# Kernel tuning notes

Hardware: AMD Instinct MI355X
Metric: run time of the kernel (lower is better)

Reference implementation:

```python
import jax, jax.numpy as jnp
import numpy as np

H = 1024      # hidden_size
I = 4096      # intermediate_size
E = 8         # num_experts
TOP_K = 2
LB_COEF = 0.01


def setup_inputs() -> dict:
    key = jax.random.key(0)
    ks = jax.random.split(key, 8)
    s_h = 1.0 / np.sqrt(H)
    s_i = 1.0 / np.sqrt(I)
    return {
        "x": jax.random.normal(ks[0], (2, 2048, H), dtype=jnp.float32),
        "Wr": jax.random.normal(ks[1], (H, E), dtype=jnp.float32) * s_h,
        "br": jnp.zeros((E,), dtype=jnp.float32),
        "W1": jax.random.normal(ks[2], (E, H, I), dtype=jnp.float32) * s_h,
        "b1": jnp.zeros((E, I), dtype=jnp.float32),
        "W2": jax.random.normal(ks[3], (E, I, H), dtype=jnp.float32) * s_i,
        "b2": jnp.zeros((E, H), dtype=jnp.float32),
    }


def _moe_forward(x, Wr, br, W1, b1, W2, b2):
    B, S, Hd = x.shape
    x_flat = x.reshape(-1, Hd)                      # [T, H]
    T = x_flat.shape[0]

    # ---- Router: softmax probs, top-k, renormalize ----
    logits = x_flat @ Wr + br                       # [T, E]
    probs = jax.nn.softmax(logits, axis=-1)         # [T, E]
    topk_w, topk_idx = jax.lax.top_k(probs, TOP_K)  # [T, K]
    topk_w = topk_w / jnp.sum(topk_w, axis=-1, keepdims=True)

    # ---- Load-balance aux loss (switch-style) ----
    onehot = jax.nn.one_hot(topk_idx, E, dtype=x.dtype)   # [T, K, E]
    frac_tokens = onehot.mean(axis=(0, 1))                 # [E]
    frac_probs = probs.mean(axis=0)                        # [E]
    aux_loss = E * jnp.sum(frac_tokens * frac_probs) * LB_COEF

    # combine_weights[t, e] = routing weight of expert e for token t (0 if unselected)
    combine = jnp.sum(topk_w[..., None] * onehot, axis=1)  # [T, E]

    # ---- Experts: dense per-expert FFN, weighted combine ----
    out = jnp.zeros_like(x_flat)
    for e in range(E):
        h = jax.nn.gelu(x_flat @ W1[e] + b1[e])            # [T, I]
        y = h @ W2[e] + b2[e]                              # [T, H]
        out = out + y * combine[:, e:e + 1]
    return out.reshape(B, S, Hd), aux_loss


def reference(x, Wr, br, W1, b1, W2, b2):
    return _moe_forward(x, Wr, br, W1, b1, W2, b2)
```

## Files before the change

### kernel.cpp

```cpp
#include <hip/hip_runtime.h>
#include <hip/hip_bf16.h>

#define HD 1024
#define ID 4096
#define NE 8
#define NT 4096
#define NSLOT (NT*2)

typedef __attribute__((ext_vector_type(4))) float f32x4;
typedef __attribute__((ext_vector_type(8))) short bf16x8;
typedef __attribute__((ext_vector_type(4))) unsigned int u32x4;
typedef __attribute__((ext_vector_type(2))) unsigned int u32x2;
typedef unsigned short u16;

__device__ __forceinline__ u16 f2b(float f) {
  __hip_bfloat16 h = __float2bfloat16(f);
  return __builtin_bit_cast(unsigned short, h);
}
__device__ __forceinline__ unsigned int pack2(float a, float b) {
  return (unsigned int)f2b(a) | ((unsigned int)f2b(b) << 16);
}
__device__ __forceinline__ void gload16(const void* g, void* l) {
  __builtin_amdgcn_global_load_lds(
      (const __attribute__((address_space(1))) unsigned int*)g,
      (__attribute__((address_space(3))) unsigned int*)l, 16, 0, 0);
}
__device__ __forceinline__ float gelu_tanh(float v) {
  float c = v + 0.044715f * v * v * v;
  return 0.5f * v * (1.0f + tanhf(0.7978845608028654f * c));
}

__global__ void k_convert_x(const float* __restrict__ x, u16* __restrict__ xb) {
  int i = blockIdx.x * 256 + threadIdx.x;
  const f32x4* x4 = (const f32x4*)x;
  f32x4 a = x4[2 * i], b = x4[2 * i + 1];
  u32x4 r;
  r[0] = pack2(a[0], a[1]); r[1] = pack2(a[2], a[3]);
  r[2] = pack2(b[0], b[1]); r[3] = pack2(b[2], b[3]);
  ((u32x4*)xb)[i] = r;
}

__global__ __launch_bounds__(256) void k_transpose_bf16(
    const float* __restrict__ src, u16* __restrict__ dst, int R, int C) {
  __shared__ float tile[64][65];
  int e = blockIdx.z;
  int c0 = blockIdx.x * 64;
  int r0 = blockIdx.y * 64;
  int t = threadIdx.x;
  const float* s = src + (size_t)e * R * C;
#pragma unroll
  for (int i = 0; i < 16; ++i) {
    int r = i * 4 + (t >> 6);
    tile[r][t & 63] = s[(size_t)(r0 + r) * C + c0 + (t & 63)];
  }
  __syncthreads();
  u16* d = dst + (size_t)e * R * C;
#pragma unroll
  for (int i = 0; i < 4; ++i) {
    int c = i * 16 + (t >> 4);
    int rb = (t & 15) * 4;
    u32x2 p;
    p[0] = pack2(tile[rb + 0][c], tile[rb + 1][c]);
    p[1] = pack2(tile[rb + 2][c], tile[rb + 3][c]);
    *(u32x2*)&d[(size_t)(c0 + c) * R + r0 + rb] = p;
  }
}

__global__ __launch_bounds__(256) void k_router(
    const float* __restrict__ x, const float* __restrict__ Wr,
    const float* __restrict__ br, int* __restrict__ cnt,
    int* __restrict__ slotE, int* __restrict__ slotLoc,
    float* __restrict__ slotW, float* __restrict__ probsAll) {
  __shared__ float wrt[NE * HD];
  int t = threadIdx.x;
  for (int i = t; i < NE * HD; i += 256) wrt[(i & 7) * HD + (i >> 3)] = Wr[i];
  __syncthreads();
  int wave = t >> 6, lane = t & 63;
  int token = blockIdx.x * 4 + wave;
  const float* xr = x + (size_t)token * HD;
  float acc[NE] = {0, 0, 0, 0, 0, 0, 0, 0};
#pragma unroll 4
  for (int j = 0; j < 16; ++j) {
    int h = j * 64 + lane;
    float xv = xr[h];
#pragma unroll
    for (int e = 0; e < NE; ++e) acc[e] += xv * wrt[e * HD + h];
  }
#pragma unroll
  for (int d = 1; d < 64; d <<= 1) {
#pragma unroll
    for (int e = 0; e < NE; ++e) acc[e] += __shfl_xor(acc[e], d, 64);
  }
  if (lane == 0) {
    float lg[NE], p[NE];
    float m = -1e30f;
#pragma unroll
    for (int e = 0; e < NE; ++e) { lg[e] = acc[e] + br[e]; m = fmaxf(m, lg[e]); }
    float s = 0.f;
#pragma unroll
    for (int e = 0; e < NE; ++e) { p[e] = expf(lg[e] - m); s += p[e]; }
    float inv = 1.0f / s;
    int i1 = 0, i2 = -1;
    float v1 = -1.f, v2 = -1.f;
#pragma unroll
    for (int e = 0; e < NE; ++e) {
      p[e] *= inv;
      probsAll[token * NE + e] = p[e];
      if (p[e] > v1) { v2 = v1; i2 = i1; v1 = p[e]; i1 = e; }
      else if (p[e] > v2) { v2 = p[e]; i2 = e; }
    }
    float wsum = v1 + v2;
    int l1 = atomicAdd(&cnt[i1], 1);
    int l2 = atomicAdd(&cnt[i2], 1);
    slotE[token * 2] = i1;     slotLoc[token * 2] = l1;     slotW[token * 2] = v1 / wsum;
    slotE[token * 2 + 1] = i2; slotLoc[token * 2 + 1] = l2; slotW[token * 2 + 1] = v2 / wsum;
  }
}

__global__ __launch_bounds__(256) void k_psum(const float* __restrict__ probsAll,
                                              float* __restrict__ psumG) {
  __shared__ float red[256];
  int t = threadIdx.x;
  int base = blockIdx.x * 128;
  float s = 0.f;
  for (int i = t >> 3; i < 128; i += 32) s += probsAll[(base + i) * NE + (t & 7)];
  red[t] = s;
  __syncthreads();
  for (int st = 128; st >= 8; st >>= 1) {
    if (t < st) red[t] += red[t + st];
    __syncthreads();
  }
  if (t < 8) atomicAdd(&psumG[t], red[t]);
}

__global__ void k_finalize(const float* __restrict__ psumG, const int* __restrict__ cnt,
                           int* __restrict__ off, float* __restrict__ out_aux) {
  if (threadIdx.x == 0) {
    int o = 0;
    float a = 0.f;
    for (int e = 0; e < NE; ++e) {
      off[e] = o;
      o += cnt[e];
      a += ((float)cnt[e] / (float)NSLOT) * (psumG[e] / (float)NT);
    }
    off[NE] = o;
    out_aux[0] = (float)NE * a * 0.01f;
  }
}

__global__ void k_scatter(const int* __restrict__ slotE, const int* __restrict__ slotLoc,
                          const float* __restrict__ slotW, const int* __restrict__ off,
                          int* __restrict__ rowTok, float* __restrict__ rowW) {
  int i = blockIdx.x * 256 + threadIdx.x;
  int pos = off[slotE[i]] + slotLoc[i];
  if (pos < 0) pos = 0;
  if (pos >= NSLOT) pos = NSLOT - 1;
  rowTok[pos] = i >> 1;
  rowW[pos] = slotW[i];
}

#define STG(bf) do { \
    _Pragma("unroll") \
    for (int i_ = 0; i_ < 4; ++i_) { \
      gload16(aSrc[i_], &As[bf][dstc[i_]]); \
      gload16(bSrc[i_], &Bs[bf][dstc[i_]]); \
      aSrc[i_] += 64; bSrc[i_] += 64; \
    } \
  } while (0)

__global__ __launch_bounds__(512, 1) void k_gemm1(
    const u16* __restrict__ xb, const u16* __restrict__ w1t,
    const float* __restrict__ b1, u16* __restrict__ hbuf,
    const int* __restrict__ cnt, const int* __restrict__ off,
    const int* __restrict__ rowTok) {
  int bid = blockIdx.x;
  int e = bid >> 8;
  int m0 = ((bid >> 4) & 15) * 256;
  int n0 = (bid & 15) * 256;
  int ce = cnt[e];
  if (m0 >= ce) return;
  int oe = off[e];
  __shared__ u16 As[2][256 * 64];
  __shared__ u16 Bs[2][256 * 64];
  __shared__ int rtok[256];
  int t = threadIdx.x;
  if (t < 256) {
    int r = m0 + t;
    if (r >= ce) r = ce - 1;
    int tok = rowTok[oe + r];
    rtok[t] = (tok < 0) ? 0 : (tok >= NT ? NT - 1 : tok);
  }
  __syncthreads();
  const u16* aSrc[4];
  const u16* bSrc[4];
  int dstc[4];
  const u16* bb = w1t + (size_t)e * ID * HD + (size_t)n0 * HD;
#pragma unroll
  for (int i = 0; i < 4; ++i) {
    int c = t + 512 * i;
    int row = c >> 3, slot = c & 7, j = slot ^ (row & 7);
    aSrc[i] = xb + (size_t)rtok[row] * HD + j * 8;
    bSrc[i] = bb + (size_t)row * HD + j * 8;
    dstc[i] = c * 8;
  }
  int lane = t & 63, wave = t >> 6;
  int wr = wave >> 2, wc = wave & 3;
  f32x4 acc[8][4] = {};
  const int NK = HD / 64;
  STG(0);
  STG(1);
  for (int kt = 0; kt < NK; ++kt) {
    if (kt + 1 < NK) asm volatile("s_waitcnt vmcnt(8)" ::: "memory");
    else             asm volatile("s_waitcnt vmcnt(0)" ::: "memory");
    __builtin_amdgcn_s_barrier();
    int cb = kt & 1;
#pragma unroll
    for (int kk = 0; kk < 2; ++kk) {
      bf16x8 af[8], bv[4];
#pragma unroll
      for (int mm = 0; mm < 8; ++mm) {
        int ra = wr * 128 + mm * 16 + (lane & 15);
        int slot = (kk * 4 + (lane >> 4)) ^ (ra & 7);
        af[mm] = *(const bf16x8*)&As[cb][ra * 64 + slot * 8];
      }
#pragma unroll
      for (int nn = 0; nn < 4; ++nn) {
        int rb = wc * 64 + nn * 16 + (lane & 15);
        int slot = (kk * 4 + (lane >> 4)) ^ (rb & 7);
        bv[nn] = *(const bf16x8*)&Bs[cb][rb * 64 + slot * 8];
      }
#pragma unroll
      for (int mm = 0; mm < 8; ++mm)
#pragma unroll
        for (int nn = 0; nn < 4; ++nn)
          acc[mm][nn] = __builtin_amdgcn_mfma_f32_16x16x32_bf16(af[mm], bv[nn], acc[mm][nn], 0, 0, 0);
    }
    if (kt + 2 < NK) {
      __builtin_amdgcn_s_barrier();
      STG(kt & 1);
    }
  }
  const float* b1e = b1 + (size_t)e * ID + n0;
#pragma unroll
  for (int nn = 0; nn < 4; ++nn) {
    int col = wc * 64 + nn * 16 + (lane & 15);
    float bias = b1e[col];
#pragma unroll
    for (int mm = 0; mm < 8; ++mm) {
      int lr0 = wr * 128 + mm * 16 + (lane >> 4) * 4;
#pragma unroll
      for (int r = 0; r < 4; ++r) {
        int grow = m0 + lr0 + r;
        if (grow < ce) {
          float v = acc[mm][nn][r] + bias;
          hbuf[(size_t)(oe + grow) * ID + n0 + col] = f2b(gelu_tanh(v));
        }
      }
    }
  }
}

__global__ __launch_bounds__(512, 1) void k_gemm2(
    const u16* __restrict__ hbuf, const u16* __restrict__ w2t,
    const float* __restrict__ b2, float* __restrict__ out,
    const int* __restrict__ cnt, const int* __restrict__ off,
    const int* __restrict__ rowTok, const float* __restrict__ rowW) {
  int bid = blockIdx.x;
  int e = bid >> 7;
  int m0 = ((bid >> 3) & 15) * 256;
  int n0 = ((bid >> 1) & 3) * 256;
  int ks = bid & 1;
  int ce = cnt[e];
  if (m0 >= ce) return;
  int oe = off[e];
  int k0 = ks * (ID / 2);
  __shared__ u16 As[2][256 * 64];
  __shared__ u16 Bs[2][256 * 64];
  __shared__ int rtok[256];
  __shared__ float rw[256];
  int t = threadIdx.x;
  if (t < 256) {
    int r = m0 + t;
    int rc = (r < ce) ? r : ce - 1;
    int tok = rowTok[oe + rc];
    rtok[t] = (tok < 0) ? 0 : (tok >= NT ? NT - 1 : tok);
    rw[t] = (r < ce) ? rowW[oe + r] : 0.0f;
  }
  __syncthreads();
  const u16* aSrc[4];
  const u16* bSrc[4];
  int dstc[4];
  const u16* bb = w2t + (size_t)e * HD * ID + (size_t)n0 * ID + k0;
#pragma unroll
  for (int i = 0; i < 4; ++i) {
    int c = t + 512 * i;
    int row = c >> 3, slot = c & 7, j = slot ^ (row & 7);
    int rA = m0 + row; if (rA >= ce) rA = ce - 1;
    aSrc[i] = hbuf + (size_t)(oe + rA) * ID + k0 + j * 8;
    bSrc[i] = bb + (size_t)row * ID + j * 8;
    dstc[i] = c * 8;
  }
  int lane = t & 63, wave = t >> 6;
  int wr = wave >> 2, wc = wave & 3;
  f32x4 acc[8][4] = {};
  const int NK = (ID / 2) / 64;
  STG(0);
  STG(1);
  for (int kt = 0; kt < NK; ++kt) {
    if (kt + 1 < NK) asm volatile("s_waitcnt vmcnt(8)" ::: "memory");
    else             asm volatile("s_waitcnt vmcnt(0)" ::: "memory");
    __builtin_amdgcn_s_barrier();
    int cb = kt & 1;
#pragma unroll
    for (int kk = 0; kk < 2; ++kk) {
      bf16x8 af[8], bv[4];
#pragma unroll
      for (int mm = 0; mm < 8; ++mm) {
        int ra = wr * 128 + mm * 16 + (lane & 15);
        int slot = (kk * 4 + (lane >> 4)) ^ (ra & 7);
        af[mm] = *(const bf16x8*)&As[cb][ra * 64 + slot * 8];
      }
#pragma unroll
      for (int nn = 0; nn < 4; ++nn) {
        int rb = wc * 64 + nn * 16 + (lane & 15);
        int slot = (kk * 4 + (lane >> 4)) ^ (rb & 7);
        bv[nn] = *(const bf16x8*)&Bs[cb][rb * 64 + slot * 8];
      }
#pragma unroll
      for (int mm = 0; mm < 8; ++mm)
#pragma unroll
        for (int nn = 0; nn < 4; ++nn)
          acc[mm][nn] = __builtin_amdgcn_mfma_f32_16x16x32_bf16(af[mm], bv[nn], acc[mm][nn], 0, 0, 0);
    }
    if (kt + 2 < NK) {
      __builtin_amdgcn_s_barrier();
      STG(kt & 1);
    }
  }
  const float* b2e = b2 + (size_t)e * HD + n0;
#pragma unroll
  for (int nn = 0; nn < 4; ++nn) {
    int col = wc * 64 + nn * 16 + (lane & 15);
    float bias = (ks == 0) ? b2e[col] : 0.0f;
#pragma unroll
    for (int mm = 0; mm < 8; ++mm) {
      int lr0 = wr * 128 + mm * 16 + (lane >> 4) * 4;
#pragma unroll
      for (int r = 0; r < 4; ++r) {
        int lr = lr0 + r;
        int grow = m0 + lr;
        if (grow < ce) {
          float v = (acc[mm][nn][r] + bias) * rw[lr];
          atomicAdd(&out[(size_t)rtok[lr] * HD + n0 + col], v);
        }
      }
    }
  }
}

extern "C" void kernel_launch(void* const* d_in, const int* in_sizes, int n_in,
                              void* d_out, int out_size, void* d_ws, size_t ws_size,
                              hipStream_t stream) {
  const float* x  = (const float*)d_in[0];
  const float* Wr = (const float*)d_in[1];
  const float* br = (const float*)d_in[2];
  const float* W1 = (const float*)d_in[3];
  const float* b1 = (const float*)d_in[4];
  const float* W2 = (const float*)d_in[5];
  const float* b2 = (const float*)d_in[6];
  float* out = (float*)d_out;

  char* ws = (char*)d_ws;
  size_t o = 0;
  auto alloc = [&](size_t bytes) {
    void* p = ws + o;
    o = (o + bytes + 255) & ~(size_t)255;
    return p;
  };
  u16* xb    = (u16*)alloc((size_t)NT * HD * 2);
  u16* w1t   = (u16*)alloc((size_t)NE * ID * HD * 2);
  u16* w2t   = (u16*)alloc((size_t)NE * ID * HD * 2);
  u16* hbuf  = (u16*)alloc((size_t)NSLOT * ID * 2);
  int* cnt     = (int*)alloc(NE * 4);
  float* psumG = (float*)alloc(NE * 4);
  int* off     = (int*)alloc(16 * 4);
  int* slotE   = (int*)alloc(NSLOT * 4);
  int* slotLoc = (int*)alloc(NSLOT * 4);
  float* slotW = (float*)alloc(NSLOT * 4);
  int* rowTok  = (int*)alloc(NSLOT * 4);
  float* rowW  = (float*)alloc(NSLOT * 4);
  float* probsAll = (float*)alloc((size_t)NT * NE * 4);

  if (ws_size < o) return;

  hipMemsetAsync(cnt, 0, NE * 4, stream);
  hipMemsetAsync(psumG, 0, NE * 4, stream);
  hipMemsetAsync(out, 0, (size_t)out_size * 4, stream);
  k_convert_x<<<(NT * HD / 8) / 256, 256, 0, stream>>>(x, xb);
  k_transpose_bf16<<<dim3(ID / 64, HD / 64, NE), 256, 0, stream>>>(W1, w1t, HD, ID);
  k_transpose_bf16<<<dim3(HD / 64, ID / 64, NE), 256, 0, stream>>>(W2, w2t, ID, HD);
  k_router<<<NT / 4, 256, 0, stream>>>(x, Wr, br, cnt, slotE, slotLoc, slotW, probsAll);
  k_psum<<<32, 256, 0, stream>>>(probsAll, psumG);
  k_finalize<<<1, 64, 0, stream>>>(psumG, cnt, off, out + (size_t)NT * HD);
  k_scatter<<<NSLOT / 256, 256, 0, stream>>>(slotE, slotLoc, slotW, off, rowTok, rowW);
  k_gemm1<<<NE * 16 * 16, 512, 0, stream>>>(xb, w1t, b1, hbuf, cnt, off, rowTok);
  k_gemm2<<<NE * 16 * 4 * 2, 512, 0, stream>>>(hbuf, w2t, b2, out, cnt, off, rowTok, rowW);
}
```

Baseline: 581.7 us.

## Restructure GEMM k-loop into phased LDS reads and MFMA bursts with priority

Replaces the k-loop body in both expert GEMMs with a four-phase schedule. Each phase loads a half-set of A fragments from LDS, waits on lgkmcnt, and issues a 16-MFMA burst under raised wave priority, with scheduling barriers and a workgroup barrier between phases. The global-to-LDS prefetch of the next tile is now issued at the top of each step instead of two tiles ahead at the end. This is meant to interleave LDS traffic with MFMA work across waves and to use fewer fragment registers. The cost is more barriers per k-step and only one tile of global prefetch lead.

```diff
diff --git a/kernel.cpp b/kernel.cpp
--- a/kernel.cpp
+++ b/kernel.cpp
@@ -166,6 +166,49 @@
       gload16(bSrc[i_], &Bs[bf][dstc[i_]]); \
       aSrc[i_] += 64; bSrc[i_] += 64; \
     } \
+  } while (0)
+
+#define PH_READ_B(KK) \
+  _Pragma("unroll") for (int nn = 0; nn < 4; ++nn) { \
+    int rb = wc * 64 + nn * 16 + (lane & 15); \
+    int slot = ((KK) * 4 + (lane >> 4)) ^ (rb & 7); \
+    bv[nn] = *(const bf16x8*)&Bs[cb][rb * 64 + slot * 8]; \
+  }
+#define PH_READ_A(KK, MLO) \
+  _Pragma("unroll") for (int m = 0; m < 4; ++m) { \
+    int ra = wr * 128 + ((MLO) + m) * 16 + (lane & 15); \
+    int slot = ((KK) * 4 + (lane >> 4)) ^ (ra & 7); \
+    af[m] = *(const bf16x8*)&As[cb][ra * 64 + slot * 8]; \
+  }
+#define PH_MFMA(MLO) do { \
+    asm volatile("s_waitcnt lgkmcnt(0)" ::: "memory"); \
+    __builtin_amdgcn_sched_barrier(0); \
+    __builtin_amdgcn_s_setprio(1); \
+    _Pragma("unroll") for (int m = 0; m < 4; ++m) \
+      _Pragma("unroll") for (int nn = 0; nn < 4; ++nn) \
+        acc[(MLO) + m][nn] = __builtin_amdgcn_mfma_f32_16x16x32_bf16(af[m], bv[nn], acc[(MLO) + m][nn], 0, 0, 0); \
+    __builtin_amdgcn_s_setprio(0); \
+    __builtin_amdgcn_sched_barrier(0); \
+    __builtin_amdgcn_s_barrier(); \
+    __builtin_amdgcn_sched_barrier(0); \
+  } while (0)
+
+#define KSTEP_BODY(NKVAL) do { \
+    int cb = kt & 1; \
+    if (kt + 1 < (NKVAL)) { \
+      STG(cb ^ 1); \
+      asm volatile("s_waitcnt vmcnt(8)" ::: "memory"); \
+    } else { \
+      asm volatile("s_waitcnt vmcnt(0)" ::: "memory"); \
+    } \
+    __builtin_amdgcn_sched_barrier(0); \
+    __builtin_amdgcn_s_barrier(); \
+    __builtin_amdgcn_sched_barrier(0); \
+    bf16x8 af[4], bv[4]; \
+    PH_READ_B(0); PH_READ_A(0, 0); PH_MFMA(0); \
+    PH_READ_A(0, 4); PH_MFMA(4); \
+    PH_READ_B(1); PH_READ_A(1, 0); PH_MFMA(0); \
+    PH_READ_A(1, 4); PH_MFMA(4); \
   } while (0)
 
 __global__ __launch_bounds__(512, 1) void k_gemm1(
@@ -208,37 +251,8 @@
   f32x4 acc[8][4] = {};
   const int NK = HD / 64;
   STG(0);
-  STG(1);
   for (int kt = 0; kt < NK; ++kt) {
-    if (kt + 1 < NK) asm volatile("s_waitcnt vmcnt(8)" ::: "memory");
-    else             asm volatile("s_waitcnt vmcnt(0)" ::: "memory");
-    __builtin_amdgcn_s_barrier();
-    int cb = kt & 1;
-#pragma unroll
-    for (int kk = 0; kk < 2; ++kk) {
-      bf16x8 af[8], bv[4];
-#pragma unroll
-      for (int mm = 0; mm < 8; ++mm) {
-        int ra = wr * 128 + mm * 16 + (lane & 15);
-        int slot = (kk * 4 + (lane >> 4)) ^ (ra & 7);
-        af[mm] = *(const bf16x8*)&As[cb][ra * 64 + slot * 8];
-      }
-#pragma unroll
-      for (int nn = 0; nn < 4; ++nn) {
-        int rb = wc * 64 + nn * 16 + (lane & 15);
-        int slot = (kk * 4 + (lane >> 4)) ^ (rb & 7);
-        bv[nn] = *(const bf16x8*)&Bs[cb][rb * 64 + slot * 8];
-      }
-#pragma unroll
-      for (int mm = 0; mm < 8; ++mm)
-#pragma unroll
-        for (int nn = 0; nn < 4; ++nn)
-          acc[mm][nn] = __builtin_amdgcn_mfma_f32_16x16x32_bf16(af[mm], bv[nn], acc[mm][nn], 0, 0, 0);
-    }
-    if (kt + 2 < NK) {
-      __builtin_amdgcn_s_barrier();
-      STG(kt & 1);
-    }
+    KSTEP_BODY(NK);
   }
   const float* b1e = b1 + (size_t)e * ID + n0;
 #pragma unroll
@@ -305,37 +319,8 @@
   f32x4 acc[8][4] = {};
   const int NK = (ID / 2) / 64;
   STG(0);
-  STG(1);
   for (int kt = 0; kt < NK; ++kt) {
-    if (kt + 1 < NK) asm volatile("s_waitcnt vmcnt(8)" ::: "memory");
-    else             asm volatile("s_waitcnt vmcnt(0)" ::: "memory");
-    __builtin_amdgcn_s_barrier();
-    int cb = kt & 1;
-#pragma unroll
-    for (int kk = 0; kk < 2; ++kk) {
-      bf16x8 af[8], bv[4];
-#pragma unroll
-      for (int mm = 0; mm < 8; ++mm) {
-        int ra = wr * 128 + mm * 16 + (lane & 15);
-        int slot = (kk * 4 + (lane >> 4)) ^ (ra & 7);
-        af[mm] = *(const bf16x8*)&As[cb][ra * 64 + slot * 8];
-      }
-#pragma unroll
-      for (int nn = 0; nn < 4; ++nn) {
-        int rb = wc * 64 + nn * 16 + (lane & 15);
-        int slot = (kk * 4 + (lane >> 4)) ^ (rb & 7);
-        bv[nn] = *(const bf16x8*)&Bs[cb][rb * 64 + slot * 8];
-      }
-#pragma unroll
-      for (int mm = 0; mm < 8; ++mm)
-#pragma unroll
-        for (int nn = 0; nn < 4; ++nn)
-          acc[mm][nn] = __builtin_amdgcn_mfma_f32_16x16x32_bf16(af[mm], bv[nn], acc[mm][nn], 0, 0, 0);
-    }
-    if (kt + 2 < NK) {
-      __builtin_amdgcn_s_barrier();
-      STG(kt & 1);
-    }
+    KSTEP_BODY(NK);
   }
   const float* b2e = b2 + (size_t)e * HD + n0;
 #pragma unroll
```

New measurement: 631.0 us. +8.5%, slower.

## Triple-buffer GEMM k-tiles with one barrier, fuse x conversion and psum into router

Applied to the files above, without the earlier changes.

Both expert GEMMs now stage K=32 tiles in a three-slot LDS ring instead of two K=64 buffers. This lets the second barrier per iteration go while keeping two tiles of loads in flight, with a new XOR swizzle for the narrower tiles. The router also writes the bf16 copy of x and reduces the softmax probability sums per block through shared-memory atomics, which removes the separate convert and psum kernels and the probs buffer. The trade-off is half the MFMA work per barrier and more loop iterations, plus float atomics that make the aux-loss summation order nondeterministic.

```diff
diff --git a/kernel.cpp b/kernel.cpp
--- a/kernel.cpp
+++ b/kernel.cpp
@@ -28,16 +28,6 @@
 __device__ __forceinline__ float gelu_tanh(float v) {
   float c = v + 0.044715f * v * v * v;
   return 0.5f * v * (1.0f + tanhf(0.7978845608028654f * c));
-}
-
-__global__ void k_convert_x(const float* __restrict__ x, u16* __restrict__ xb) {
-  int i = blockIdx.x * 256 + threadIdx.x;
-  const f32x4* x4 = (const f32x4*)x;
-  f32x4 a = x4[2 * i], b = x4[2 * i + 1];
-  u32x4 r;
-  r[0] = pack2(a[0], a[1]); r[1] = pack2(a[2], a[3]);
-  r[2] = pack2(b[0], b[1]); r[3] = pack2(b[2], b[3]);
-  ((u32x4*)xb)[i] = r;
 }
 
 __global__ __launch_bounds__(256) void k_transpose_bf16(
@@ -70,19 +60,24 @@
     const float* __restrict__ x, const float* __restrict__ Wr,
     const float* __restrict__ br, int* __restrict__ cnt,
     int* __restrict__ slotE, int* __restrict__ slotLoc,
-    float* __restrict__ slotW, float* __restrict__ probsAll) {
+    float* __restrict__ slotW, float* __restrict__ psumG,
+    u16* __restrict__ xb) {
   __shared__ float wrt[NE * HD];
+  __shared__ float blkp[NE];
   int t = threadIdx.x;
+  if (t < NE) blkp[t] = 0.0f;
   for (int i = t; i < NE * HD; i += 256) wrt[(i & 7) * HD + (i >> 3)] = Wr[i];
   __syncthreads();
   int wave = t >> 6, lane = t & 63;
   int token = blockIdx.x * 4 + wave;
   const float* xr = x + (size_t)token * HD;
+  u16* xbr = xb + (size_t)token * HD;
   float acc[NE] = {0, 0, 0, 0, 0, 0, 0, 0};
 #pragma unroll 4
   for (int j = 0; j < 16; ++j) {
     int h = j * 64 + lane;
     float xv = xr[h];
+    xbr[h] = f2b(xv);
 #pragma unroll
     for (int e = 0; e < NE; ++e) acc[e] += xv * wrt[e * HD + h];
   }
@@ -105,7 +100,7 @@
 #pragma unroll
     for (int e = 0; e < NE; ++e) {
       p[e] *= inv;
-      probsAll[token * NE + e] = p[e];
+      atomicAdd(&blkp[e], p[e]);
       if (p[e] > v1) { v2 = v1; i2 = i1; v1 = p[e]; i1 = e; }
       else if (p[e] > v2) { v2 = p[e]; i2 = e; }
     }
@@ -115,22 +110,8 @@
     slotE[token * 2] = i1;     slotLoc[token * 2] = l1;     slotW[token * 2] = v1 / wsum;
     slotE[token * 2 + 1] = i2; slotLoc[token * 2 + 1] = l2; slotW[token * 2 + 1] = v2 / wsum;
   }
-}
-
-__global__ __launch_bounds__(256) void k_psum(const float* __restrict__ probsAll,
-                                              float* __restrict__ psumG) {
-  __shared__ float red[256];
-  int t = threadIdx.x;
-  int base = blockIdx.x * 128;
-  float s = 0.f;
-  for (int i = t >> 3; i < 128; i += 32) s += probsAll[(base + i) * NE + (t & 7)];
-  red[t] = s;
-  __syncthreads();
-  for (int st = 128; st >= 8; st >>= 1) {
-    if (t < st) red[t] += red[t + st];
-    __syncthreads();
-  }
-  if (t < 8) atomicAdd(&psumG[t], red[t]);
+  __syncthreads();
+  if (t < NE) atomicAdd(&psumG[t], blkp[t]);
 }
 
 __global__ void k_finalize(const float* __restrict__ psumG, const int* __restrict__ cnt,
@@ -160,12 +141,11 @@
 }
 
 #define STG(bf) do { \
-    _Pragma("unroll") \
-    for (int i_ = 0; i_ < 4; ++i_) { \
-      gload16(aSrc[i_], &As[bf][dstc[i_]]); \
-      gload16(bSrc[i_], &Bs[bf][dstc[i_]]); \
-      aSrc[i_] += 64; bSrc[i_] += 64; \
-    } \
+    gload16(srcA0, &As[bf][c0 * 8]); \
+    gload16(srcA1, &As[bf][c1 * 8]); \
+    gload16(srcB0, &Bs[bf][c0 * 8]); \
+    gload16(srcB1, &Bs[bf][c1 * 8]); \
+    srcA0 += 32; srcA1 += 32; srcB0 += 32; srcB1 += 32; \
   } while (0)
 
 __global__ __launch_bounds__(512, 1) void k_gemm1(
@@ -180,8 +160,8 @@
   int ce = cnt[e];
   if (m0 >= ce) return;
   int oe = off[e];
-  __shared__ u16 As[2][256 * 64];
-  __shared__ u16 Bs[2][256 * 64];
+  __shared__ u16 As[3][256 * 32];
+  __shared__ u16 Bs[3][256 * 32];
   __shared__ int rtok[256];
   int t = threadIdx.x;
   if (t < 256) {
@@ -191,54 +171,48 @@
     rtok[t] = (tok < 0) ? 0 : (tok >= NT ? NT - 1 : tok);
   }
   __syncthreads();
-  const u16* aSrc[4];
-  const u16* bSrc[4];
-  int dstc[4];
+  int c0 = t, c1 = t + 512;
+  int js0 = (c0 & 3) ^ ((c0 >> 3) & 3);
+  int js1 = (c1 & 3) ^ ((c1 >> 3) & 3);
+  const u16* srcA0 = xb + (size_t)rtok[c0 >> 2] * HD + js0 * 8;
+  const u16* srcA1 = xb + (size_t)rtok[c1 >> 2] * HD + js1 * 8;
   const u16* bb = w1t + (size_t)e * ID * HD + (size_t)n0 * HD;
-#pragma unroll
-  for (int i = 0; i < 4; ++i) {
-    int c = t + 512 * i;
-    int row = c >> 3, slot = c & 7, j = slot ^ (row & 7);
-    aSrc[i] = xb + (size_t)rtok[row] * HD + j * 8;
-    bSrc[i] = bb + (size_t)row * HD + j * 8;
-    dstc[i] = c * 8;
-  }
+  const u16* srcB0 = bb + (size_t)(c0 >> 2) * HD + js0 * 8;
+  const u16* srcB1 = bb + (size_t)(c1 >> 2) * HD + js1 * 8;
   int lane = t & 63, wave = t >> 6;
   int wr = wave >> 2, wc = wave & 3;
   f32x4 acc[8][4] = {};
-  const int NK = HD / 64;
+  const int NK = HD / 32;
   STG(0);
   STG(1);
+  int rb = 0;
   for (int kt = 0; kt < NK; ++kt) {
-    if (kt + 1 < NK) asm volatile("s_waitcnt vmcnt(8)" ::: "memory");
+    if (kt + 1 < NK) asm volatile("s_waitcnt vmcnt(4)" ::: "memory");
     else             asm volatile("s_waitcnt vmcnt(0)" ::: "memory");
     __builtin_amdgcn_s_barrier();
-    int cb = kt & 1;
-#pragma unroll
-    for (int kk = 0; kk < 2; ++kk) {
-      bf16x8 af[8], bv[4];
-#pragma unroll
-      for (int mm = 0; mm < 8; ++mm) {
-        int ra = wr * 128 + mm * 16 + (lane & 15);
-        int slot = (kk * 4 + (lane >> 4)) ^ (ra & 7);
-        af[mm] = *(const bf16x8*)&As[cb][ra * 64 + slot * 8];
-      }
-#pragma unroll
-      for (int nn = 0; nn < 4; ++nn) {
-        int rb = wc * 64 + nn * 16 + (lane & 15);
-        int slot = (kk * 4 + (lane >> 4)) ^ (rb & 7);
-        bv[nn] = *(const bf16x8*)&Bs[cb][rb * 64 + slot * 8];
-      }
-#pragma unroll
-      for (int mm = 0; mm < 8; ++mm)
-#pragma unroll
-        for (int nn = 0; nn < 4; ++nn)
-          acc[mm][nn] = __builtin_amdgcn_mfma_f32_16x16x32_bf16(af[mm], bv[nn], acc[mm][nn], 0, 0, 0);
-    }
+    bf16x8 af[8], bv[4];
+#pragma unroll
+    for (int mm = 0; mm < 8; ++mm) {
+      int ra = wr * 128 + mm * 16 + (lane & 15);
+      int slot = (lane >> 4) ^ ((ra >> 1) & 3);
+      af[mm] = *(const bf16x8*)&As[rb][ra * 32 + slot * 8];
+    }
+#pragma unroll
+    for (int nn = 0; nn < 4; ++nn) {
+      int rbr = wc * 64 + nn * 16 + (lane & 15);
+      int slot = (lane >> 4) ^ ((rbr >> 1) & 3);
+      bv[nn] = *(const bf16x8*)&Bs[rb][rbr * 32 + slot * 8];
+    }
+#pragma unroll
+    for (int mm = 0; mm < 8; ++mm)
+#pragma unroll
+      for (int nn = 0; nn < 4; ++nn)
+        acc[mm][nn] = __builtin_amdgcn_mfma_f32_16x16x32_bf16(af[mm], bv[nn], acc[mm][nn], 0, 0, 0);
     if (kt + 2 < NK) {
-      __builtin_amdgcn_s_barrier();
-      STG(kt & 1);
-    }
+      int sb = rb + 2; if (sb >= 3) sb -= 3;
+      STG(sb);
+    }
+    rb = (rb == 2) ? 0 : rb + 1;
   }
   const float* b1e = b1 + (size_t)e * ID + n0;
 #pragma unroll
@@ -274,8 +248,8 @@
   if (m0 >= ce) return;
   int oe = off[e];
   int k0 = ks * (ID / 2);
-  __shared__ u16 As[2][256 * 64];
-  __shared__ u16 Bs[2][256 * 64];
+  __shared__ u16 As[3][256 * 32];
+  __shared__ u16 Bs[3][256 * 32];
   __shared__ int rtok[256];
   __shared__ float rw[256];
   int t = threadIdx.x;
@@ -287,55 +261,50 @@
     rw[t] = (r < ce) ? rowW[oe + r] : 0.0f;
   }
   __syncthreads();
-  const u16* aSrc[4];
-  const u16* bSrc[4];
-  int dstc[4];
+  int c0 = t, c1 = t + 512;
+  int js0 = (c0 & 3) ^ ((c0 >> 3) & 3);
+  int js1 = (c1 & 3) ^ ((c1 >> 3) & 3);
+  int rA0 = m0 + (c0 >> 2); if (rA0 >= ce) rA0 = ce - 1;
+  int rA1 = m0 + (c1 >> 2); if (rA1 >= ce) rA1 = ce - 1;
+  const u16* srcA0 = hbuf + (size_t)(oe + rA0) * ID + k0 + js0 * 8;
+  const u16* srcA1 = hbuf + (size_t)(oe + rA1) * ID + k0 + js1 * 8;
   const u16* bb = w2t + (size_t)e * HD * ID + (size_t)n0 * ID + k0;
-#pragma unroll
-  for (int i = 0; i < 4; ++i) {
-    int c = t + 512 * i;
-    int row = c >> 3, slot = c & 7, j = slot ^ (row & 7);
-    int rA = m0 + row; if (rA >= ce) rA = ce - 1;
-    aSrc[i] = hbuf + (size_t)(oe + rA) * ID + k0 + j * 8;
-    bSrc[i] = bb + (size_t)row * ID + j * 8;
-    dstc[i] = c * 8;
-  }
+  const u16* srcB0 = bb + (size_t)(c0 >> 2) * ID + js0 * 8;
+  const u16* srcB1 = bb + (size_t)(c1 >> 2) * ID + js1 * 8;
   int lane = t & 63, wave = t >> 6;
   int wr = wave >> 2, wc = wave & 3;
   f32x4 acc[8][4] = {};
-  const int NK = (ID / 2) / 64;
+  const int NK = (ID / 2) / 32;
   STG(0);
   STG(1);
+  int rb = 0;
   for (int kt = 0; kt < NK; ++kt) {
-    if (kt + 1 < NK) asm volatile("s_waitcnt vmcnt(8)" ::: "memory");
+    if (kt + 1 < NK) asm volatile("s_waitcnt vmcnt(4)" ::: "memory");
     else             asm volatile("s_waitcnt vmcnt(0)" ::: "memory");
     __builtin_amdgcn_s_barrier();
-    int cb = kt & 1;
-#pragma unroll
-    for (int kk = 0; kk < 2; ++kk) {
-      bf16x8 af[8], bv[4];
-#pragma unroll
-      for (int mm = 0; mm < 8; ++mm) {
-        int ra = wr * 128 + mm * 16 + (lane & 15);
-        int slot = (kk * 4 + (lane >> 4)) ^ (ra & 7);
-        af[mm] = *(const bf16x8*)&As[cb][ra * 64 + slot * 8];
-      }
-#pragma unroll
-      for (int nn = 0; nn < 4; ++nn) {
-        int rb = wc * 64 + nn * 16 + (lane & 15);
-        int slot = (kk * 4 + (lane >> 4)) ^ (rb & 7);
-        bv[nn] = *(const bf16x8*)&Bs[cb][rb * 64 + slot * 8];
-      }
-#pragma unroll
-      for (int mm = 0; mm < 8; ++mm)
-#pragma unroll
-        for (int nn = 0; nn < 4; ++nn)
-          acc[mm][nn] = __builtin_amdgcn_mfma_f32_16x16x32_bf16(af[mm], bv[nn], acc[mm][nn], 0, 0, 0);
-    }
+    bf16x8 af[8], bv[4];
+#pragma unroll
+    for (int mm = 0; mm < 8; ++mm) {
+      int ra = wr * 128 + mm * 16 + (lane & 15);
+      int slot = (lane >> 4) ^ ((ra >> 1) & 3);
+      af[mm] = *(const bf16x8*)&As[rb][ra * 32 + slot * 8];
+    }
+#pragma unroll
+    for (int nn = 0; nn < 4; ++nn) {
+      int rbr = wc * 64 + nn * 16 + (lane & 15);
+      int slot = (lane >> 4) ^ ((rbr >> 1) & 3);
+      bv[nn] = *(const bf16x8*)&Bs[rb][rbr * 32 + slot * 8];
+    }
+#pragma unroll
+    for (int mm = 0; mm < 8; ++mm)
+#pragma unroll
+      for (int nn = 0; nn < 4; ++nn)
+        acc[mm][nn] = __builtin_amdgcn_mfma_f32_16x16x32_bf16(af[mm], bv[nn], acc[mm][nn], 0, 0, 0);
     if (kt + 2 < NK) {
-      __builtin_amdgcn_s_barrier();
-      STG(kt & 1);
-    }
+      int sb = rb + 2; if (sb >= 3) sb -= 3;
+      STG(sb);
+    }
+    rb = (rb == 2) ? 0 : rb + 1;
   }
   const float* b2e = b2 + (size_t)e * HD + n0;
 #pragma unroll
@@ -389,18 +358,15 @@
   float* slotW = (float*)alloc(NSLOT * 4);
   int* rowTok  = (int*)alloc(NSLOT * 4);
   float* rowW  = (float*)alloc(NSLOT * 4);
-  float* probsAll = (float*)alloc((size_t)NT * NE * 4);
 
   if (ws_size < o) return;
 
   hipMemsetAsync(cnt, 0, NE * 4, stream);
   hipMemsetAsync(psumG, 0, NE * 4, stream);
   hipMemsetAsync(out, 0, (size_t)out_size * 4, stream);
-  k_convert_x<<<(NT * HD / 8) / 256, 256, 0, stream>>>(x, xb);
   k_transpose_bf16<<<dim3(ID / 64, HD / 64, NE), 256, 0, stream>>>(W1, w1t, HD, ID);
   k_transpose_bf16<<<dim3(HD / 64, ID / 64, NE), 256, 0, stream>>>(W2, w2t, ID, HD);
-  k_router<<<NT / 4, 256, 0, stream>>>(x, Wr, br, cnt, slotE, slotLoc, slotW, probsAll);
-  k_psum<<<32, 256, 0, stream>>>(probsAll, psumG);
+  k_router<<<NT / 4, 256, 0, stream>>>(x, Wr, br, cnt, slotE, slotLoc, slotW, psumG, xb);
   k_finalize<<<1, 64, 0, stream>>>(psumG, cnt, off, out + (size_t)NT * HD);
   k_scatter<<<NSLOT / 256, 256, 0, stream>>>(slotE, slotLoc, slotW, off, rowTok, rowW);
   k_gemm1<<<NE * 16 * 16, 512, 0, stream>>>(xb, w1t, b1, hbuf, cnt, off, rowTok);
```

Result: faster. 559.8 us (-3.8%).
